# Kernel tuning notes

Hardware: AMD Instinct MI355X
Metric: run time of the kernel (lower is better)

## Reference

```python
import jax, jax.numpy as jnp
import numpy as np

H = 512          # hidden_size
DEPTH = 6        # number of tanh layers
N = 8192         # collocation points
DT = 0.1         # uniform time step
MIN_ALPHA = 0.6  # initial_params['min_alpha']


def _xavier(k, fi, fo):
    lim = np.sqrt(6.0 / (fi + fo))
    return jax.random.uniform(k, (fi, fo), minval=-lim, maxval=lim, dtype=jnp.float32)


def _raw(x):
    # inverse-softplus style init used by EpiPINN: raw = x + log(-expm1(-x))
    return jnp.array([x + np.log(-np.expm1(-x))], dtype=jnp.float32)


def setup_inputs() -> dict:
    key = jax.random.key(0)
    ks = jax.random.split(key, DEPTH + 2)
    W_in = _xavier(ks[0], 1, H)
    b_in = jnp.zeros((H,), jnp.float32)
    Wh = jnp.stack([_xavier(ks[1 + l], H, H) for l in range(DEPTH - 1)])  # [DEPTH-1,H,H]
    bh = jnp.zeros((DEPTH - 1, H), jnp.float32)
    W_out = _xavier(ks[DEPTH], H, 5)
    b_out = jnp.zeros((5,), jnp.float32)
    t = (jnp.arange(N, dtype=jnp.float32) * DT).reshape(N, 1)
    return {
        't': t,
        'W_in': W_in, 'b_in': b_in, 'Wh': Wh, 'bh': bh,
        'W_out': W_out, 'b_out': b_out,
        'raw_beta': _raw(0.3), 'raw_sigma': _raw(0.2),
        'raw_gamma': _raw(0.1), 'raw_mu': _raw(0.05),
        'z_alpha': jnp.array([0.0], dtype=jnp.float32),
    }


def _forward_all(t, W_in, b_in, Wh, bh, W_out, b_out,
                 raw_beta, raw_sigma, raw_gamma, raw_mu, z_alpha):
    # --- PINN MLP: 1 -> H (tanh) x DEPTH -> 5, softmax over components ---
    h = jnp.tanh(t @ W_in + b_in)
    for l in range(Wh.shape[0]):  # static small loop over layers
        h = jnp.tanh(h @ Wh[l] + bh[l])
    y = jax.nn.softmax(h @ W_out + b_out, axis=1)  # [n,5]

    alpha = MIN_ALPHA + (1.0 - MIN_ALPHA) * jax.nn.sigmoid(z_alpha[0])
    beta = jax.nn.softplus(raw_beta[0])
    sigma = jax.nn.softplus(raw_sigma[0])
    gamma = jax.nn.softplus(raw_gamma[0])
    mu = jax.nn.softplus(raw_mu[0])

    # --- Caputo L1 fractional derivative for all 5 components at once ---
    n = y.shape[0]
    dpsi = y[1:] - y[:-1]  # [n-1,5] first differences
    rs = jnp.arange(n - 1, dtype=y.dtype)
    rs_safe = jnp.where(rs == 0, 1.0, rs)  # avoid 0**x grad nan; value unchanged
    ws = (rs + 1.0) ** (1.0 - alpha) - jnp.where(rs == 0, 0.0, rs_safe ** (1.0 - alpha))
    C = DT ** (-alpha) / jnp.exp(jax.lax.lgamma(2.0 - alpha))
    ii = jnp.arange(n - 1)
    idx = ii[:, None] - ii[None, :]
    A = jnp.where(idx >= 0, ws[jnp.clip(idx, 0)], 0.0)  # lower-triangular Toeplitz [n-1,n-1]
    dfrac = jnp.concatenate([jnp.zeros((1, 5), y.dtype), C * (A @ dpsi)], axis=0)  # [n,5]

    # --- SEIRD right-hand side and physics residual ---
    s, e, i, r, d = (y[:, k:k + 1] for k in range(5))
    living = 1.0 - d
    inf_term = beta * s * i / living
    f = jnp.concatenate([
        -inf_term,
        inf_term - sigma * e,
        sigma * e - (gamma + mu) * i,
        gamma * i,
        mu * i,
    ], axis=1)  # [n,5]
    return jnp.mean((dfrac - f) ** 2)


def reference(t, W_in, b_in, Wh, bh, W_out, b_out,
              raw_beta, raw_sigma, raw_gamma, raw_mu, z_alpha):
    return _forward_all(t, W_in, b_in, Wh, bh, W_out, b_out,
                        raw_beta, raw_sigma, raw_gamma, raw_mu, z_alpha)
```

## Files before the change

### kernel.cpp

```cpp
#include <hip/hip_runtime.h>
#include <math.h>

typedef short short8v __attribute__((ext_vector_type(8)));
typedef float float4v __attribute__((ext_vector_type(4)));

#define N_PTS 8192
#define HDIM  512
#define NHID  5
#define KSTR  1024
#define NCH   16

#define OFF_XA    0ull
#define OFF_XB    16777216ull
#define OFF_WT    33554432ull
#define OFF_Y     38797312ull
#define OFF_DPSI  38961152ull
#define OFF_WSW   39124992ull
#define OFF_PART  39157760ull
#define OFF_BPART 41779200ull

__device__ __forceinline__ unsigned short f2bf(float x) {
  unsigned u = __builtin_bit_cast(unsigned, x);
  u += 0x7FFFu + ((u >> 16) & 1u);
  return (unsigned short)(u >> 16);
}
__device__ __forceinline__ float bf2f(unsigned short h) {
  unsigned u = ((unsigned)h) << 16;
  return __builtin_bit_cast(float, u);
}

#define GLOAD16(gsrc, ldst) \
  __builtin_amdgcn_global_load_lds( \
      (const __attribute__((address_space(1))) void*)(gsrc), \
      (__attribute__((address_space(3))) void*)(ldst), 16, 0, 0)

__global__ void wprep_kernel(const float* __restrict__ Wh,
                             unsigned short* __restrict__ WT) {
  __shared__ float tile[32][33];
  int l = blockIdx.z;
  int kb = blockIdx.x;
  int n0 = blockIdx.y * 32;
  int j = threadIdx.x & 31, i8 = threadIdx.x >> 5;
  const float* W = Wh + (size_t)l * HDIM * HDIM;
#pragma unroll
  for (int q = 0; q < 4; ++q)
    tile[i8 + 8 * q][j] = W[(size_t)(kb * 32 + i8 + 8 * q) * HDIM + n0 + j];
  __syncthreads();
#pragma unroll
  for (int q = 0; q < 4; ++q) {
    int n = n0 + i8 + 8 * q;
    float v = tile[j][i8 + 8 * q];
    unsigned short h = f2bf(v);
    unsigned short lo = f2bf(v - bf2f(h));
    size_t o = ((size_t)l * HDIM + n) * KSTR + kb * 64 + j;
    WT[o] = h; WT[o + 32] = lo;
  }
}

__global__ void layer0_kernel(const float* __restrict__ t,
                              const float* __restrict__ Win,
                              const float* __restrict__ bin,
                              unsigned short* __restrict__ X) {
  int gid = blockIdx.x * blockDim.x + threadIdx.x;
  int row = gid >> 7;
  int jq  = (gid & 127) << 2;
  float tv = t[row];
  float4 w = *(const float4*)(Win + jq);
  float4 b = *(const float4*)(bin + jq);
  float v[4];
  v[0] = tanhf(tv * w.x + b.x); v[1] = tanhf(tv * w.y + b.y);
  v[2] = tanhf(tv * w.z + b.z); v[3] = tanhf(tv * w.w + b.w);
  ushort4 h4, l4;
  h4.x = f2bf(v[0]); l4.x = f2bf(v[0] - bf2f(h4.x));
  h4.y = f2bf(v[1]); l4.y = f2bf(v[1] - bf2f(h4.y));
  h4.z = f2bf(v[2]); l4.z = f2bf(v[2] - bf2f(h4.z));
  h4.w = f2bf(v[3]); l4.w = f2bf(v[3] - bf2f(h4.w));
  size_t o = (size_t)row * KSTR + (jq >> 5) * 64 + (jq & 31);
  *(ushort4*)(X + o) = h4;
  *(ushort4*)(X + o + 32) = l4;
}

__global__ __launch_bounds__(256) void gemm_split_kernel(
    const unsigned short* __restrict__ A,
    const unsigned short* __restrict__ Bt,
    const float* __restrict__ bias,
    unsigned short* __restrict__ C) {
  __shared__ __align__(16) short lds[3][12288];
  const int tid = threadIdx.x;
  const int lane = tid & 63, w = tid >> 6;
  const int wc = w;
  const int r0 = blockIdx.x * 64, c0 = blockIdx.y * 128;
  const int rl = lane & 15, kgrp = lane >> 4;

  float4v acc[4][2];
#pragma unroll
  for (int i = 0; i < 4; ++i)
#pragma unroll
    for (int j = 0; j < 2; ++j) acc[i][j] = (float4v){0.f, 0.f, 0.f, 0.f};

  auto stage = [&](int b, int kt) {
    const int kbase = kt * 64;
#pragma unroll
    for (int i = 0; i < 2; ++i) {
      int c = i * 256 + tid;
      int row = c >> 3, m = c & 7;
      int gs = m ^ (row & 7);
      GLOAD16(A + (size_t)(r0 + row) * KSTR + kbase + gs * 8,
              &lds[b][(i * 256 + w * 64) * 8]);
    }
#pragma unroll
    for (int i = 0; i < 4; ++i) {
      int c = i * 256 + tid;
      int col = c >> 3, m = c & 7;
      int gs = m ^ (col & 7);
      GLOAD16(Bt + (size_t)(c0 + col) * KSTR + kbase + gs * 8,
              &lds[b][4096 + (i * 256 + w * 64) * 8]);
    }
  };

  stage(0, 0);
  stage(1, 1);
  asm volatile("s_waitcnt vmcnt(6)" ::: "memory");
  __builtin_amdgcn_s_barrier();
  asm volatile("" ::: "memory");

#pragma unroll 1
  for (int kt = 0; kt < 16; ++kt) {
    if (kt < 14) stage((kt + 2) % 3, kt + 2);
    const short* bufc = lds[kt % 3];
    short8v ahi[4], alo[4], bhi[2], blo[2];
#pragma unroll
    for (int mi = 0; mi < 4; ++mi) {
      int row = mi * 16 + rl;
      int sh = kgrp ^ (row & 7);
      int sl = (kgrp + 4) ^ (row & 7);
      ahi[mi] = *(const short8v*)&bufc[row * 64 + sh * 8];
      alo[mi] = *(const short8v*)&bufc[row * 64 + sl * 8];
    }
#pragma unroll
    for (int ni = 0; ni < 2; ++ni) {
      int col = wc * 32 + ni * 16 + rl;
      int sh = kgrp ^ (col & 7);
      int sl = (kgrp + 4) ^ (col & 7);
      bhi[ni] = *(const short8v*)&bufc[4096 + col * 64 + sh * 8];
      blo[ni] = *(const short8v*)&bufc[4096 + col * 64 + sl * 8];
    }
    __builtin_amdgcn_s_setprio(1);
#pragma unroll
    for (int mi = 0; mi < 4; ++mi)
#pragma unroll
      for (int ni = 0; ni < 2; ++ni)
        acc[mi][ni] = __builtin_amdgcn_mfma_f32_16x16x32_bf16(ahi[mi], bhi[ni], acc[mi][ni], 0, 0, 0);
#pragma unroll
    for (int mi = 0; mi < 4; ++mi)
#pragma unroll
      for (int ni = 0; ni < 2; ++ni)
        acc[mi][ni] = __builtin_amdgcn_mfma_f32_16x16x32_bf16(ahi[mi], blo[ni], acc[mi][ni], 0, 0, 0);
#pragma unroll
    for (int mi = 0; mi < 4; ++mi)
#pragma unroll
      for (int ni = 0; ni < 2; ++ni)
        acc[mi][ni] = __builtin_amdgcn_mfma_f32_16x16x32_bf16(alo[mi], bhi[ni], acc[mi][ni], 0, 0, 0);
    __builtin_amdgcn_s_setprio(0);
    if (kt < 15) {
      if (kt < 14) asm volatile("s_waitcnt vmcnt(6)" ::: "memory");
      else         asm volatile("s_waitcnt vmcnt(0)" ::: "memory");
      __builtin_amdgcn_s_barrier();
      asm volatile("" ::: "memory");
    }
  }

  float bcol[2];
#pragma unroll
  for (int ni = 0; ni < 2; ++ni) bcol[ni] = bias[c0 + wc * 32 + ni * 16 + rl];
#pragma unroll
  for (int mi = 0; mi < 4; ++mi)
#pragma unroll
    for (int ni = 0; ni < 2; ++ni)
#pragma unroll
      for (int r = 0; r < 4; ++r) {
        int row = r0 + mi * 16 + kgrp * 4 + r;
        int col = c0 + wc * 32 + ni * 16 + rl;
        float v = tanhf(acc[mi][ni][r] + bcol[ni]);
        unsigned short h = f2bf(v);
        unsigned short lo = f2bf(v - bf2f(h));
        size_t o = (size_t)row * KSTR + (col >> 5) * 64 + (col & 31);
        C[o] = h; C[o + 32] = lo;
      }
}

__global__ void outlayer_kernel(const unsigned short* __restrict__ X,
                                const float* __restrict__ Wout,
                                const float* __restrict__ bout,
                                float* __restrict__ y) {
  int wid  = threadIdx.x >> 6;
  int lane = threadIdx.x & 63;
  int row  = blockIdx.x * 4 + wid;
  size_t o = (size_t)row * KSTR + (lane >> 2) * 64 + (lane & 3) * 8;
  short8v hv = *(const short8v*)(X + o);
  short8v lv = *(const short8v*)(X + o + 32);
  const float* wrp = Wout + lane * 40;
  float acc[5] = {0.f, 0.f, 0.f, 0.f, 0.f};
#pragma unroll
  for (int e = 0; e < 8; ++e) {
    float h = bf2f((unsigned short)hv[e]) + bf2f((unsigned short)lv[e]);
#pragma unroll
    for (int c = 0; c < 5; ++c) acc[c] += h * wrp[e * 5 + c];
  }
#pragma unroll
  for (int c = 0; c < 5; ++c)
    for (int off = 32; off; off >>= 1) acc[c] += __shfl_down(acc[c], off);
  if (lane == 0) {
    float l[5], m = -1e30f;
#pragma unroll
    for (int c = 0; c < 5; ++c) { l[c] = acc[c] + bout[c]; m = fmaxf(m, l[c]); }
    float s = 0.f;
#pragma unroll
    for (int c = 0; c < 5; ++c) { l[c] = expf(l[c] - m); s += l[c]; }
    float inv = 1.f / s;
#pragma unroll
    for (int c = 0; c < 5; ++c) y[row * 5 + c] = l[c] * inv;
  }
}

__global__ void prep_caputo_kernel(const float* __restrict__ z_alpha,
                                   const float* __restrict__ y,
                                   float* __restrict__ wsw,
                                   float* __restrict__ dpsi) {
  int g = blockIdx.x * blockDim.x + threadIdx.x;
  if (g < (N_PTS - 1) * 5) dpsi[g] = y[g + 5] - y[g];
  if (g < N_PTS - 1) {
    double z = (double)z_alpha[0];
    double alpha = 0.6 + 0.4 / (1.0 + exp(-z));
    double p = 1.0 - alpha;
    double w = pow((double)g + 1.0, p) - (g == 0 ? 0.0 : pow((double)g, p));
    wsw[g] = (float)w;
  }
}

__global__ __launch_bounds__(256) void conv_kernel(
    const float* __restrict__ dpsi, const float* __restrict__ wsw,
    float* __restrict__ part) {
  __shared__ float dps[256][8];
  __shared__ float wsl[512];
  int tid = threadIdx.x;
  int r0  = blockIdx.x * 256;
  int ch  = blockIdx.y;
  int r   = r0 + tid;
  float acc[5] = {0.f, 0.f, 0.f, 0.f, 0.f};

  for (int t4 = 0; t4 < 2; ++t4) {
    int j0 = ch * 512 + t4 * 256;
    if (j0 > r0 + 254) break;
    __syncthreads();
    {
      const float* dr = dpsi + (size_t)(j0 + tid) * 5;
      dps[tid][0] = dr[0]; dps[tid][1] = dr[1]; dps[tid][2] = dr[2];
      dps[tid][3] = dr[3]; dps[tid][4] = dr[4];
    }
    int base = r0 - j0 - 256;
#pragma unroll
    for (int s = 0; s < 2; ++s) {
      int i = tid + s * 256;
      int src = base + i;
      wsl[i] = (src >= 0 && src < N_PTS - 1) ? wsw[src] : 0.f;
    }
    __syncthreads();
    int widx = tid + 255;
#pragma unroll 4
    for (int jj = 0; jj < 256; ++jj) {
      float w = wsl[widx - jj];
      float4 d4 = *(const float4*)&dps[jj][0];
      float d5 = dps[jj][4];
      acc[0] += w * d4.x; acc[1] += w * d4.y; acc[2] += w * d4.z;
      acc[3] += w * d4.w; acc[4] += w * d5;
    }
  }
  float* p = part + ((size_t)ch * N_PTS + r) * 5;
  p[0] = acc[0]; p[1] = acc[1]; p[2] = acc[2]; p[3] = acc[3]; p[4] = acc[4];
}

__device__ __forceinline__ float softplusf_(float x) {
  return x > 20.f ? x : log1pf(expf(x));
}

__global__ void combine_kernel(const float* __restrict__ y,
                               const float* __restrict__ part,
                               const float* __restrict__ rb, const float* __restrict__ rs,
                               const float* __restrict__ rg, const float* __restrict__ rm,
                               const float* __restrict__ za,
                               float* __restrict__ bpart) {
  __shared__ float red[128];
  int tid = threadIdx.x;
  int row = blockIdx.x * 128 + tid;

  float beta  = softplusf_(rb[0]);
  float sigma = softplusf_(rs[0]);
  float gamma = softplusf_(rg[0]);
  float mu    = softplusf_(rm[0]);
  double z = (double)za[0];
  double alpha = 0.6 + 0.4 / (1.0 + exp(-z));
  float C = (float)(pow(0.1, -alpha) / tgamma(2.0 - alpha));

  float df[5];
  if (row == 0) {
    df[0] = df[1] = df[2] = df[3] = df[4] = 0.f;
  } else {
#pragma unroll
    for (int c = 0; c < 5; ++c) {
      float s = 0.f;
#pragma unroll
      for (int ch = 0; ch < NCH; ++ch)
        s += part[((size_t)ch * N_PTS + row) * 5 + c];
      df[c] = C * s;
    }
  }
  float yv[5];
#pragma unroll
  for (int c = 0; c < 5; ++c) yv[c] = y[row * 5 + c];
  float living = 1.f - yv[4];
  float inf_t = beta * yv[0] * yv[2] / living;
  float f[5];
  f[0] = -inf_t;
  f[1] = inf_t - sigma * yv[1];
  f[2] = sigma * yv[1] - (gamma + mu) * yv[2];
  f[3] = gamma * yv[2];
  f[4] = mu * yv[2];
  float s = 0.f;
#pragma unroll
  for (int c = 0; c < 5; ++c) { float d = df[c] - f[c]; s += d * d; }

  red[tid] = s;
  __syncthreads();
  for (int off = 64; off; off >>= 1) {
    if (tid < off) red[tid] += red[tid + off];
    __syncthreads();
  }
  if (tid == 0) bpart[blockIdx.x] = red[0];
}

__global__ void finish_kernel(const float* __restrict__ bpart, float* __restrict__ out) {
  if (threadIdx.x == 0) {
    float s = 0.f;
    for (int i = 0; i < 64; ++i) s += bpart[i];
    out[0] = s / (float)(N_PTS * 5);
  }
}

extern "C" void kernel_launch(void* const* d_in, const int* in_sizes, int n_in,
                              void* d_out, int out_size, void* d_ws, size_t ws_size,
                              hipStream_t stream) {
  const float* t     = (const float*)d_in[0];
  const float* W_in  = (const float*)d_in[1];
  const float* b_in  = (const float*)d_in[2];
  const float* Wh    = (const float*)d_in[3];
  const float* bh    = (const float*)d_in[4];
  const float* W_out = (const float*)d_in[5];
  const float* b_out = (const float*)d_in[6];
  const float* rbta  = (const float*)d_in[7];
  const float* rsig  = (const float*)d_in[8];
  const float* rgam  = (const float*)d_in[9];
  const float* rmu   = (const float*)d_in[10];
  const float* zalp  = (const float*)d_in[11];

  char* wsb = (char*)d_ws;
  unsigned short* XA = (unsigned short*)(wsb + OFF_XA);
  unsigned short* XB = (unsigned short*)(wsb + OFF_XB);
  unsigned short* WT = (unsigned short*)(wsb + OFF_WT);
  float* y     = (float*)(wsb + OFF_Y);
  float* dpsi  = (float*)(wsb + OFF_DPSI);
  float* wsw   = (float*)(wsb + OFF_WSW);
  float* part  = (float*)(wsb + OFF_PART);
  float* bpart = (float*)(wsb + OFF_BPART);
  float* out   = (float*)d_out;

  wprep_kernel<<<dim3(16, 16, 5), 256, 0, stream>>>(Wh, WT);

  layer0_kernel<<<N_PTS * 128 / 256, 256, 0, stream>>>(t, W_in, b_in, XA);

  for (int l = 0; l < NHID; ++l) {
    const unsigned short* in = (l & 1) ? XB : XA;
    unsigned short*      oub = (l & 1) ? XA : XB;
    gemm_split_kernel<<<dim3(N_PTS / 64, HDIM / 128), 256, 0, stream>>>(
        in, WT + (size_t)l * HDIM * KSTR, bh + (size_t)l * HDIM, oub);
  }

  outlayer_kernel<<<N_PTS / 4, 256, 0, stream>>>(XB, W_out, b_out, y);

  prep_caputo_kernel<<<160, 256, 0, stream>>>(zalp, y, wsw, dpsi);

  conv_kernel<<<dim3(N_PTS / 256, NCH), 256, 0, stream>>>(dpsi, wsw, part);

  combine_kernel<<<N_PTS / 128, 128, 0, stream>>>(y, part, rbta, rsig, rgam, rmu,
                                                  zalp, bpart);
  finish_kernel<<<1, 64, 0, stream>>>(bpart, out);
  (void)in_sizes; (void)n_in; (void)out_size; (void)ws_size;
}
```

Before: 138.6 us.

## Merge prep kernels, fold Caputo prep into conv, use 8-wave GEMM blocks

Merges the weight-transpose and layer-0 kernels into one launch. The Caputo prep kernel is removed: the conv kernel now computes first differences from y and the power-law weights in double precision inline. Separately, the GEMM moves to 512 threads with a 2x4 wave grid, halving per-wave accumulator tiles to raise occupancy and latency hiding. The trade-off is redundant double-precision pow evaluation in every conv block and less per-wave reuse in the GEMM.

```diff
diff --git a/kernel.cpp b/kernel.cpp
--- a/kernel.cpp
+++ b/kernel.cpp
@@ -14,8 +14,6 @@
 #define OFF_XB    16777216ull
 #define OFF_WT    33554432ull
 #define OFF_Y     38797312ull
-#define OFF_DPSI  38961152ull
-#define OFF_WSW   39124992ull
 #define OFF_PART  39157760ull
 #define OFF_BPART 41779200ull
 
@@ -34,53 +32,53 @@
       (const __attribute__((address_space(1))) void*)(gsrc), \
       (__attribute__((address_space(3))) void*)(ldst), 16, 0, 0)
 
-__global__ void wprep_kernel(const float* __restrict__ Wh,
-                             unsigned short* __restrict__ WT) {
-  __shared__ float tile[32][33];
-  int l = blockIdx.z;
-  int kb = blockIdx.x;
-  int n0 = blockIdx.y * 32;
-  int j = threadIdx.x & 31, i8 = threadIdx.x >> 5;
-  const float* W = Wh + (size_t)l * HDIM * HDIM;
-#pragma unroll
-  for (int q = 0; q < 4; ++q)
-    tile[i8 + 8 * q][j] = W[(size_t)(kb * 32 + i8 + 8 * q) * HDIM + n0 + j];
-  __syncthreads();
-#pragma unroll
-  for (int q = 0; q < 4; ++q) {
-    int n = n0 + i8 + 8 * q;
-    float v = tile[j][i8 + 8 * q];
-    unsigned short h = f2bf(v);
-    unsigned short lo = f2bf(v - bf2f(h));
-    size_t o = ((size_t)l * HDIM + n) * KSTR + kb * 64 + j;
-    WT[o] = h; WT[o + 32] = lo;
-  }
-}
-
-__global__ void layer0_kernel(const float* __restrict__ t,
-                              const float* __restrict__ Win,
-                              const float* __restrict__ bin,
-                              unsigned short* __restrict__ X) {
-  int gid = blockIdx.x * blockDim.x + threadIdx.x;
-  int row = gid >> 7;
-  int jq  = (gid & 127) << 2;
-  float tv = t[row];
-  float4 w = *(const float4*)(Win + jq);
-  float4 b = *(const float4*)(bin + jq);
-  float v[4];
-  v[0] = tanhf(tv * w.x + b.x); v[1] = tanhf(tv * w.y + b.y);
-  v[2] = tanhf(tv * w.z + b.z); v[3] = tanhf(tv * w.w + b.w);
-  ushort4 h4, l4;
-  h4.x = f2bf(v[0]); l4.x = f2bf(v[0] - bf2f(h4.x));
-  h4.y = f2bf(v[1]); l4.y = f2bf(v[1] - bf2f(h4.y));
-  h4.z = f2bf(v[2]); l4.z = f2bf(v[2] - bf2f(h4.z));
-  h4.w = f2bf(v[3]); l4.w = f2bf(v[3] - bf2f(h4.w));
-  size_t o = (size_t)row * KSTR + (jq >> 5) * 64 + (jq & 31);
-  *(ushort4*)(X + o) = h4;
-  *(ushort4*)(X + o + 32) = l4;
-}
-
-__global__ __launch_bounds__(256) void gemm_split_kernel(
+__global__ void prep_kernel(const float* __restrict__ Wh,
+                            unsigned short* __restrict__ WT,
+                            const float* __restrict__ t,
+                            const float* __restrict__ Win,
+                            const float* __restrict__ bin,
+                            unsigned short* __restrict__ X) {
+  int bid = blockIdx.x;
+  if (bid < 1280) {
+    __shared__ float tile[32][33];
+    int kb = bid & 15, n0 = ((bid >> 4) & 15) * 32, l = bid >> 8;
+    int j = threadIdx.x & 31, i8 = threadIdx.x >> 5;
+    const float* W = Wh + (size_t)l * HDIM * HDIM;
+#pragma unroll
+    for (int q = 0; q < 4; ++q)
+      tile[i8 + 8 * q][j] = W[(size_t)(kb * 32 + i8 + 8 * q) * HDIM + n0 + j];
+    __syncthreads();
+#pragma unroll
+    for (int q = 0; q < 4; ++q) {
+      int n = n0 + i8 + 8 * q;
+      float v = tile[j][i8 + 8 * q];
+      unsigned short h = f2bf(v);
+      unsigned short lo = f2bf(v - bf2f(h));
+      size_t o = ((size_t)l * HDIM + n) * KSTR + kb * 64 + j;
+      WT[o] = h; WT[o + 32] = lo;
+    }
+  } else {
+    int gid = (bid - 1280) * 256 + threadIdx.x;
+    int row = gid >> 7;
+    int jq  = (gid & 127) << 2;
+    float tv = t[row];
+    float4 w = *(const float4*)(Win + jq);
+    float4 b = *(const float4*)(bin + jq);
+    float v[4];
+    v[0] = tanhf(tv * w.x + b.x); v[1] = tanhf(tv * w.y + b.y);
+    v[2] = tanhf(tv * w.z + b.z); v[3] = tanhf(tv * w.w + b.w);
+    ushort4 h4, l4;
+    h4.x = f2bf(v[0]); l4.x = f2bf(v[0] - bf2f(h4.x));
+    h4.y = f2bf(v[1]); l4.y = f2bf(v[1] - bf2f(h4.y));
+    h4.z = f2bf(v[2]); l4.z = f2bf(v[2] - bf2f(h4.z));
+    h4.w = f2bf(v[3]); l4.w = f2bf(v[3] - bf2f(h4.w));
+    size_t o = (size_t)row * KSTR + (jq >> 5) * 64 + (jq & 31);
+    *(ushort4*)(X + o) = h4;
+    *(ushort4*)(X + o + 32) = l4;
+  }
+}
+
+__global__ __launch_bounds__(512, 4) void gemm_split_kernel(
     const unsigned short* __restrict__ A,
     const unsigned short* __restrict__ Bt,
     const float* __restrict__ bias,
@@ -88,39 +86,38 @@
   __shared__ __align__(16) short lds[3][12288];
   const int tid = threadIdx.x;
   const int lane = tid & 63, w = tid >> 6;
-  const int wc = w;
+  const int wr = w >> 2, wc = w & 3;
   const int r0 = blockIdx.x * 64, c0 = blockIdx.y * 128;
   const int rl = lane & 15, kgrp = lane >> 4;
 
-  float4v acc[4][2];
-#pragma unroll
-  for (int i = 0; i < 4; ++i)
+  float4v acc[2][2];
+#pragma unroll
+  for (int i = 0; i < 2; ++i)
 #pragma unroll
     for (int j = 0; j < 2; ++j) acc[i][j] = (float4v){0.f, 0.f, 0.f, 0.f};
 
   auto stage = [&](int b, int kt) {
     const int kbase = kt * 64;
-#pragma unroll
-    for (int i = 0; i < 2; ++i) {
-      int c = i * 256 + tid;
+    {
+      int c = tid;
       int row = c >> 3, m = c & 7;
       int gs = m ^ (row & 7);
       GLOAD16(A + (size_t)(r0 + row) * KSTR + kbase + gs * 8,
-              &lds[b][(i * 256 + w * 64) * 8]);
-    }
-#pragma unroll
-    for (int i = 0; i < 4; ++i) {
-      int c = i * 256 + tid;
+              &lds[b][(w * 64) * 8]);
+    }
+#pragma unroll
+    for (int i = 0; i < 2; ++i) {
+      int c = i * 512 + tid;
       int col = c >> 3, m = c & 7;
       int gs = m ^ (col & 7);
       GLOAD16(Bt + (size_t)(c0 + col) * KSTR + kbase + gs * 8,
-              &lds[b][4096 + (i * 256 + w * 64) * 8]);
+              &lds[b][4096 + (i * 512 + w * 64) * 8]);
     }
   };
 
   stage(0, 0);
   stage(1, 1);
-  asm volatile("s_waitcnt vmcnt(6)" ::: "memory");
+  asm volatile("s_waitcnt vmcnt(3)" ::: "memory");
   __builtin_amdgcn_s_barrier();
   asm volatile("" ::: "memory");
 
@@ -128,10 +125,10 @@
   for (int kt = 0; kt < 16; ++kt) {
     if (kt < 14) stage((kt + 2) % 3, kt + 2);
     const short* bufc = lds[kt % 3];
-    short8v ahi[4], alo[4], bhi[2], blo[2];
-#pragma unroll
-    for (int mi = 0; mi < 4; ++mi) {
-      int row = mi * 16 + rl;
+    short8v ahi[2], alo[2], bhi[2], blo[2];
+#pragma unroll
+    for (int mi = 0; mi < 2; ++mi) {
+      int row = wr * 32 + mi * 16 + rl;
       int sh = kgrp ^ (row & 7);
       int sl = (kgrp + 4) ^ (row & 7);
       ahi[mi] = *(const short8v*)&bufc[row * 64 + sh * 8];
@@ -147,23 +144,23 @@
     }
     __builtin_amdgcn_s_setprio(1);
 #pragma unroll
-    for (int mi = 0; mi < 4; ++mi)
+    for (int mi = 0; mi < 2; ++mi)
 #pragma unroll
       for (int ni = 0; ni < 2; ++ni)
         acc[mi][ni] = __builtin_amdgcn_mfma_f32_16x16x32_bf16(ahi[mi], bhi[ni], acc[mi][ni], 0, 0, 0);
 #pragma unroll
-    for (int mi = 0; mi < 4; ++mi)
+    for (int mi = 0; mi < 2; ++mi)
 #pragma unroll
       for (int ni = 0; ni < 2; ++ni)
         acc[mi][ni] = __builtin_amdgcn_mfma_f32_16x16x32_bf16(ahi[mi], blo[ni], acc[mi][ni], 0, 0, 0);
 #pragma unroll
-    for (int mi = 0; mi < 4; ++mi)
+    for (int mi = 0; mi < 2; ++mi)
 #pragma unroll
       for (int ni = 0; ni < 2; ++ni)
         acc[mi][ni] = __builtin_amdgcn_mfma_f32_16x16x32_bf16(alo[mi], bhi[ni], acc[mi][ni], 0, 0, 0);
     __builtin_amdgcn_s_setprio(0);
     if (kt < 15) {
-      if (kt < 14) asm volatile("s_waitcnt vmcnt(6)" ::: "memory");
+      if (kt < 14) asm volatile("s_waitcnt vmcnt(3)" ::: "memory");
       else         asm volatile("s_waitcnt vmcnt(0)" ::: "memory");
       __builtin_amdgcn_s_barrier();
       asm volatile("" ::: "memory");
@@ -174,12 +171,12 @@
 #pragma unroll
   for (int ni = 0; ni < 2; ++ni) bcol[ni] = bias[c0 + wc * 32 + ni * 16 + rl];
 #pragma unroll
-  for (int mi = 0; mi < 4; ++mi)
+  for (int mi = 0; mi < 2; ++mi)
 #pragma unroll
     for (int ni = 0; ni < 2; ++ni)
 #pragma unroll
       for (int r = 0; r < 4; ++r) {
-        int row = r0 + mi * 16 + kgrp * 4 + r;
+        int row = r0 + wr * 32 + mi * 16 + kgrp * 4 + r;
         int col = c0 + wc * 32 + ni * 16 + rl;
         float v = tanhf(acc[mi][ni][r] + bcol[ni]);
         unsigned short h = f2bf(v);
@@ -223,23 +220,8 @@
   }
 }
 
-__global__ void prep_caputo_kernel(const float* __restrict__ z_alpha,
-                                   const float* __restrict__ y,
-                                   float* __restrict__ wsw,
-                                   float* __restrict__ dpsi) {
-  int g = blockIdx.x * blockDim.x + threadIdx.x;
-  if (g < (N_PTS - 1) * 5) dpsi[g] = y[g + 5] - y[g];
-  if (g < N_PTS - 1) {
-    double z = (double)z_alpha[0];
-    double alpha = 0.6 + 0.4 / (1.0 + exp(-z));
-    double p = 1.0 - alpha;
-    double w = pow((double)g + 1.0, p) - (g == 0 ? 0.0 : pow((double)g, p));
-    wsw[g] = (float)w;
-  }
-}
-
 __global__ __launch_bounds__(256) void conv_kernel(
-    const float* __restrict__ dpsi, const float* __restrict__ wsw,
+    const float* __restrict__ y, const float* __restrict__ za,
     float* __restrict__ part) {
   __shared__ float dps[256][8];
   __shared__ float wsl[512];
@@ -249,21 +231,37 @@
   int r   = r0 + tid;
   float acc[5] = {0.f, 0.f, 0.f, 0.f, 0.f};
 
+  double z = (double)za[0];
+  double alpha = 0.6 + 0.4 / (1.0 + exp(-z));
+  double p = 1.0 - alpha;
+
   for (int t4 = 0; t4 < 2; ++t4) {
     int j0 = ch * 512 + t4 * 256;
     if (j0 > r0 + 254) break;
     __syncthreads();
     {
-      const float* dr = dpsi + (size_t)(j0 + tid) * 5;
-      dps[tid][0] = dr[0]; dps[tid][1] = dr[1]; dps[tid][2] = dr[2];
-      dps[tid][3] = dr[3]; dps[tid][4] = dr[4];
+      int jr = j0 + tid;
+      if (jr <= N_PTS - 2) {
+        const float* y0 = y + (size_t)jr * 5;
+        dps[tid][0] = y0[5] - y0[0]; dps[tid][1] = y0[6] - y0[1];
+        dps[tid][2] = y0[7] - y0[2]; dps[tid][3] = y0[8] - y0[3];
+        dps[tid][4] = y0[9] - y0[4];
+      } else {
+        dps[tid][0] = dps[tid][1] = dps[tid][2] = dps[tid][3] = dps[tid][4] = 0.f;
+      }
     }
     int base = r0 - j0 - 256;
 #pragma unroll
     for (int s = 0; s < 2; ++s) {
       int i = tid + s * 256;
       int src = base + i;
-      wsl[i] = (src >= 0 && src < N_PTS - 1) ? wsw[src] : 0.f;
+      float wv = 0.f;
+      if (src >= 0 && src < N_PTS - 1) {
+        double ww = pow((double)src + 1.0, p) -
+                    (src == 0 ? 0.0 : pow((double)src, p));
+        wv = (float)ww;
+      }
+      wsl[i] = wv;
     }
     __syncthreads();
     int widx = tid + 255;
@@ -276,8 +274,8 @@
       acc[3] += w * d4.w; acc[4] += w * d5;
     }
   }
-  float* p = part + ((size_t)ch * N_PTS + r) * 5;
-  p[0] = acc[0]; p[1] = acc[1]; p[2] = acc[2]; p[3] = acc[3]; p[4] = acc[4];
+  float* pp = part + ((size_t)ch * N_PTS + r) * 5;
+  pp[0] = acc[0]; pp[1] = acc[1]; pp[2] = acc[2]; pp[3] = acc[3]; pp[4] = acc[4];
 }
 
 __device__ __forceinline__ float softplusf_(float x) {
@@ -368,28 +366,22 @@
   unsigned short* XB = (unsigned short*)(wsb + OFF_XB);
   unsigned short* WT = (unsigned short*)(wsb + OFF_WT);
   float* y     = (float*)(wsb + OFF_Y);
-  float* dpsi  = (float*)(wsb + OFF_DPSI);
-  float* wsw   = (float*)(wsb + OFF_WSW);
   float* part  = (float*)(wsb + OFF_PART);
   float* bpart = (float*)(wsb + OFF_BPART);
   float* out   = (float*)d_out;
 
-  wprep_kernel<<<dim3(16, 16, 5), 256, 0, stream>>>(Wh, WT);
-
-  layer0_kernel<<<N_PTS * 128 / 256, 256, 0, stream>>>(t, W_in, b_in, XA);
+  prep_kernel<<<5376, 256, 0, stream>>>(Wh, WT, t, W_in, b_in, XA);
 
   for (int l = 0; l < NHID; ++l) {
     const unsigned short* in = (l & 1) ? XB : XA;
     unsigned short*      oub = (l & 1) ? XA : XB;
-    gemm_split_kernel<<<dim3(N_PTS / 64, HDIM / 128), 256, 0, stream>>>(
+    gemm_split_kernel<<<dim3(N_PTS / 64, HDIM / 128), 512, 0, stream>>>(
         in, WT + (size_t)l * HDIM * KSTR, bh + (size_t)l * HDIM, oub);
   }
 
   outlayer_kernel<<<N_PTS / 4, 256, 0, stream>>>(XB, W_out, b_out, y);
 
-  prep_caputo_kernel<<<160, 256, 0, stream>>>(zalp, y, wsw, dpsi);
-
-  conv_kernel<<<dim3(N_PTS / 256, NCH), 256, 0, stream>>>(dpsi, wsw, part);
+  conv_kernel<<<dim3(N_PTS / 256, NCH), 256, 0, stream>>>(y, zalp, part);
 
   combine_kernel<<<N_PTS / 128, 128, 0, stream>>>(y, part, rbta, rsig, rgam, rmu,
                                                   zalp, bpart);
```

Result: faster. 132.9 us, median of 3 (-4.1%).
